# Performance work log

Hardware: AMD Instinct MI355X
Metric: run time of the kernel (lower is better)

Reference implementation:

```python
import jax, jax.numpy as jnp
import numpy as np

N_X = 3
NE = 2048
Emin = 1.0
Emax = 100.0


def setup_inputs() -> dict:
    key = jax.random.key(0)
    k1, k2, k3, k4 = jax.random.split(key, 4)
    # log-spaced energy grid (MeV); code assumes E_grid[0] == Emin
    E_grid = jnp.logspace(np.log10(Emin), np.log10(Emax), NE, dtype=jnp.float32)
    # rates O(1), kernels small -> diagonally dominant per-step system, stable recursion
    R = 1.0 + jax.random.uniform(k1, (N_X, NE), dtype=jnp.float32)
    K = 1e-3 * jax.random.uniform(k2, (N_X, N_X, NE, NE), dtype=jnp.float32)
    S0 = jax.random.uniform(k3, (N_X,), dtype=jnp.float32)
    SC = jax.random.uniform(k4, (N_X, NE), dtype=jnp.float32)
    T = jnp.float32(0.01)
    return {"E_grid": E_grid, "R": R, "K": K, "S0": S0, "SC": SC, "T": T}


def _solve_cascade(E_grid, R, K, S0, SC, T):
    n_x, ne = R.shape
    dy = jnp.log(E_grid[-1] / Emin) / (ne - 1)

    src_last = S0 / R[:, -1]  # (N_X,) : S0[Xp] / R[Xp, -1]
    # boundary value at highest energy: FX_E0[X] = SC[X,-1]/R[X,-1] + sum_Xp K[X,Xp,-1,-1]*S0[Xp]/(R[Xp,-1]*R[X,-1])
    FX_E0 = SC[:, -1] / R[:, -1] + (K[:, :, -1, -1] @ src_last) / R[:, -1]
    F0 = jnp.zeros((n_x, ne), dtype=E_grid.dtype).at[:, -1].set(FX_E0)

    jidx = jnp.arange(ne)

    def step(F, i):
        Ki = K[:, :, i, :]  # (N_X, N_X, NE) slice at outer grid point i
        # trapezoid weights over j: dy*E[j] for i < j < NE-1, half-weight at j = NE-1, 0 elsewhere
        w = jnp.where((jidx > i) & (jidx < ne - 1), dy * E_grid, jnp.zeros((), E_grid.dtype))
        w = w.at[-1].set(0.5 * dy * E_grid[-1])
        # a[X] = SC[X,i] + sum_Xp,j Ki[X,Xp,j] * w[j] * F[Xp,j] + sum_Xp Ki[X,Xp,-1]*S0[Xp]/R[Xp,-1]
        a = SC[:, i] + jnp.einsum('xpj,pj->x', Ki, w * F) + Ki[:, :, -1] @ src_last
        # B[X,Xp] = -0.5*dy*E[i]*K[X,Xp,i,i] + R[X,i]*delta(X,Xp)
        B = -0.5 * dy * E_grid[i] * Ki[:, :, i] + jnp.diag(R[:, i])
        F = F.at[:, i].set(jnp.linalg.solve(B, a))
        return F, None

    idx = jnp.arange(ne - 2, -1, -1)  # backward sweep i = NE-2 ... 0
    F_grid, _ = jax.lax.scan(step, F0, idx)

    approx_zero = jnp.asarray(1e-200, F_grid.dtype)  # underflows to 0 in fp32, matching clamp intent
    F_grid = jnp.where(F_grid > approx_zero, F_grid, approx_zero)

    # sol: row 0 = E_grid, rows 1..N_X = spectra
    return jnp.concatenate([E_grid[None, :], F_grid], axis=0)


def reference(E_grid, R, K, S0, SC, T):
    return _solve_cascade(E_grid, R, K, S0, SC, T)
```

## Files before the change

kernel.cpp:

```cpp
#include <hip/hip_runtime.h>
#include <cstddef>
#include <cstdint>

#define NE 2048
#define NX 3
#define NROWS (NE - 1)
#define BS 64
#define BR (3 * BS)
#define NBLK 32
#define NPAIR 16


static __device__ __forceinline__ float dy_of(const float* E) {
    return logf(E[NE - 1] / E[0]) / (float)(NE - 1);
}

#define DOT4(a, b) ((a).x * (b).x + (a).y * (b).y + (a).z * (b).z + (a).w * (b).w)
#define FMA4(acc, s, b) { (acc).x += (s) * (b).x; (acc).y += (s) * (b).y; \
                          (acc).z += (s) * (b).z; (acc).w += (s) * (b).w; }

__global__ void k_init(const float* __restrict__ E, const float* __restrict__ R,
                       const float* __restrict__ K, const float* __restrict__ S0,
                       const float* __restrict__ SC,
                       float* __restrict__ out, float* __restrict__ wf,
                       float* __restrict__ acc) {
    int i = blockIdx.x * blockDim.x + threadIdx.x;
    if (i >= NE) return;
    const size_t PL = (size_t)NE * NE;
    float dy = dy_of(E);
    float wlast = 0.5f * dy * E[NE - 1];
    float srcl[NX], Fl[NX];
#pragma unroll
    for (int p = 0; p < NX; ++p) srcl[p] = S0[p] / R[p * NE + NE - 1];
#pragma unroll
    for (int x = 0; x < NX; ++x) {
        float s = SC[x * NE + NE - 1];
#pragma unroll
        for (int p = 0; p < NX; ++p)
            s += K[(size_t)(x * NX + p) * PL + (size_t)(NE - 1) * NE + (NE - 1)] * srcl[p];
        Fl[x] = s / R[x * NE + NE - 1];
    }
    out[i] = E[i];
    if (i == NE - 1) {
#pragma unroll
        for (int x = 0; x < NX; ++x) {
            out[(1 + x) * NE + i] = Fl[x] > 0.f ? Fl[x] : 0.f;
            wf[x * NE + i] = wlast * Fl[x];
            acc[x * NE + i] = 0.f;
        }
        return;
    }
#pragma unroll
    for (int x = 0; x < NX; ++x) {
        float s = SC[x * NE + i];
#pragma unroll
        for (int p = 0; p < NX; ++p)
            s += K[(size_t)(x * NX + p) * PL + (size_t)i * NE + (NE - 1)] *
                 (wlast * Fl[p] + srcl[p]);
        acc[x * NE + i] = s;
    }
}

__global__ __launch_bounds__(256) void k_tinv16(const float* __restrict__ E,
                                                const float* __restrict__ R,
                                                const float* __restrict__ K,
                                                float* __restrict__ Gs16) {
    __shared__ float4 Xs4[16][49];
    __shared__ float Kst[16][16][12];
    __shared__ float Binv[16][9];
    __shared__ float wloc[16];
    const size_t PL = (size_t)NE * NE;
    int sb = blockIdx.x;
    int i0 = sb * 16;
    int tid = threadIdx.x;
    float dy = dy_of(E);

    if (tid < 16) {
        int j = i0 + tid;
        wloc[tid] = (j < NE - 1) ? dy * E[j] : 0.f;
        int i = i0 + tid, ii = tid;
        float b00, b01, b02, b10, b11, b12, b20, b21, b22;
        if (i < NROWS) {
            float h = -0.5f * dy * E[i];
            size_t d = (size_t)i * NE + i;
            b00 = h * K[0 * PL + d] + R[0 * NE + i];
            b01 = h * K[1 * PL + d];
            b02 = h * K[2 * PL + d];
            b10 = h * K[3 * PL + d];
            b11 = h * K[4 * PL + d] + R[1 * NE + i];
            b12 = h * K[5 * PL + d];
            b20 = h * K[6 * PL + d];
            b21 = h * K[7 * PL + d];
            b22 = h * K[8 * PL + d] + R[2 * NE + i];
        } else {
            b00 = 1.f; b01 = 0.f; b02 = 0.f;
            b10 = 0.f; b11 = 1.f; b12 = 0.f;
            b20 = 0.f; b21 = 0.f; b22 = 1.f;
        }
        float C00 = b11 * b22 - b12 * b21;
        float C01 = -(b10 * b22 - b12 * b20);
        float C02 = b10 * b21 - b11 * b20;
        float C10 = -(b01 * b22 - b02 * b21);
        float C11 = b00 * b22 - b02 * b20;
        float C12 = -(b00 * b21 - b01 * b20);
        float C20 = b01 * b12 - b02 * b11;
        float C21 = -(b00 * b12 - b02 * b10);
        float C22 = b00 * b11 - b01 * b10;
        float inv = 1.f / (b00 * C00 + b01 * C01 + b02 * C02);
        Binv[ii][0] = C00 * inv; Binv[ii][1] = C10 * inv; Binv[ii][2] = C20 * inv;
        Binv[ii][3] = C01 * inv; Binv[ii][4] = C11 * inv; Binv[ii][5] = C21 * inv;
        Binv[ii][6] = C02 * inv; Binv[ii][7] = C12 * inv; Binv[ii][8] = C22 * inv;
    }
    __syncthreads();
    for (int q = tid; q < 16 * 16 * 9; q += 256) {
        int jj = q & 15;
        int ii = (q >> 4) & 15;
        int pair = q >> 8;
        Kst[ii][jj][4 * (pair / 3) + (pair % 3)] =
            K[(size_t)pair * PL + (size_t)(i0 + ii) * NE + (i0 + jj)] * wloc[jj];
    }
    __syncthreads();

    int cloc = tid >> 2, sub = tid & 3;
    if (cloc < 48) {
        for (int ii = 15; ii >= 0; --ii) {
            int i = i0 + ii;
            float v0 = 0.f, v1 = 0.f, v2 = 0.f;
            if (sub == 0) {
                v0 = (cloc == 0 * 16 + ii) ? 1.f : 0.f;
                v1 = (cloc == 1 * 16 + ii) ? 1.f : 0.f;
                v2 = (cloc == 2 * 16 + ii) ? 1.f : 0.f;
            }
            if (i < NROWS) {
                for (int jj = ii + 1 + sub; jj < 16; jj += 4) {
                    const float* kp = &Kst[ii][jj][0];
                    float4 k0 = *(const float4*)(kp);
                    float4 k1 = *(const float4*)(kp + 4);
                    float4 k2 = *(const float4*)(kp + 8);
                    float4 xv = Xs4[jj][cloc];
                    v0 += k0.x * xv.x + k0.y * xv.y + k0.z * xv.z;
                    v1 += k1.x * xv.x + k1.y * xv.y + k1.z * xv.z;
                    v2 += k2.x * xv.x + k2.y * xv.y + k2.z * xv.z;
                }
            }
            v0 += __shfl_xor(v0, 1); v0 += __shfl_xor(v0, 2);
            v1 += __shfl_xor(v1, 1); v1 += __shfl_xor(v1, 2);
            v2 += __shfl_xor(v2, 1); v2 += __shfl_xor(v2, 2);
            if (sub == 0) {
                float f0, f1, f2;
                if (i < NROWS) {
                    const float* bv = Binv[ii];
                    f0 = bv[0] * v0 + bv[1] * v1 + bv[2] * v2;
                    f1 = bv[3] * v0 + bv[4] * v1 + bv[5] * v2;
                    f2 = bv[6] * v0 + bv[7] * v1 + bv[8] * v2;
                } else {
                    f0 = v0; f1 = v1; f2 = v2;
                }
                Xs4[ii][cloc] = make_float4(f0, f1, f2, 0.f);
            }
            __builtin_amdgcn_wave_barrier();
        }
    }
    __syncthreads();
    float* Gb = Gs16 + (size_t)sb * 48 * 48;
    for (int t = tid; t < 48 * 48; t += 256) {
        int rp = t / 48, c = t % 48;
        int x = rp >> 4, ii = rp & 15;
        Gb[t] = ((const float*)&Xs4[ii][c])[x];
    }
}

__global__ __launch_bounds__(256) void k_merge48(const float* __restrict__ E,
                                                 const float* __restrict__ K,
                                                 const float* __restrict__ Gs16,
                                                 float* __restrict__ G32) {
    __shared__ float Ls[48][49], Bs[48][49], Ks[48][49], Ms[48][49];
    const size_t PL = (size_t)NE * NE;
    int q = blockIdx.x;
    int i0 = q * 32;
    int tid = threadIdx.x;
    float dy = dy_of(E);
    const float* GL = Gs16 + (size_t)(2 * q) * 2304;
    const float* GH = Gs16 + (size_t)(2 * q + 1) * 2304;
    for (int t = tid; t < 2304; t += 256) {
        int r = t / 48, c = t % 48;
        Ls[r][c] = GL[t];
        Bs[r][c] = GH[t];
        int x = r >> 4, ii = r & 15, p = c >> 4, jj = c & 15;
        int j = i0 + 16 + jj;
        float w = (j < NE - 1) ? dy * E[j] : 0.f;
        Ks[r][c] = w * K[(size_t)(x * 3 + p) * PL + (size_t)(i0 + ii) * NE + j];
    }
    __syncthreads();
    int tx = tid & 15, ty = tid >> 4;
    float m[3][3] = {};
    for (int k = 0; k < 48; ++k) {
        float a0 = Ks[ty * 3 + 0][k], a1 = Ks[ty * 3 + 1][k], a2 = Ks[ty * 3 + 2][k];
        float b0 = Bs[k][tx * 3 + 0], b1 = Bs[k][tx * 3 + 1], b2 = Bs[k][tx * 3 + 2];
        m[0][0] += a0 * b0; m[0][1] += a0 * b1; m[0][2] += a0 * b2;
        m[1][0] += a1 * b0; m[1][1] += a1 * b1; m[1][2] += a1 * b2;
        m[2][0] += a2 * b0; m[2][1] += a2 * b1; m[2][2] += a2 * b2;
    }
#pragma unroll
    for (int i = 0; i < 3; ++i)
#pragma unroll
        for (int j = 0; j < 3; ++j) Ms[ty * 3 + i][tx * 3 + j] = m[i][j];
    __syncthreads();
    float cc[3][3] = {};
    for (int k = 0; k < 48; ++k) {
        float a0 = Ls[ty * 3 + 0][k], a1 = Ls[ty * 3 + 1][k], a2 = Ls[ty * 3 + 2][k];
        float b0 = Ms[k][tx * 3 + 0], b1 = Ms[k][tx * 3 + 1], b2 = Ms[k][tx * 3 + 2];
        cc[0][0] += a0 * b0; cc[0][1] += a0 * b1; cc[0][2] += a0 * b2;
        cc[1][0] += a1 * b0; cc[1][1] += a1 * b1; cc[1][2] += a1 * b2;
        cc[2][0] += a2 * b0; cc[2][1] += a2 * b1; cc[2][2] += a2 * b2;
    }
    float* O = G32 + (size_t)q * 96 * 96;
    for (int t = tid; t < 2304; t += 256) {
        int r = t / 48, c = t % 48;
        int x = r >> 4, ii = r & 15, p = c >> 4, jj = c & 15;
        O[(size_t)(x * 32 + ii) * 96 + (p * 32 + jj)] = Ls[r][c];
        O[(size_t)(x * 32 + 16 + ii) * 96 + (p * 32 + 16 + jj)] = Bs[r][c];
        O[(size_t)(x * 32 + 16 + ii) * 96 + (p * 32 + jj)] = 0.f;
    }
#pragma unroll
    for (int i = 0; i < 3; ++i)
#pragma unroll
        for (int j = 0; j < 3; ++j) {
            int r = ty * 3 + i, c = tx * 3 + j;
            int x = r >> 4, ii = r & 15, p = c >> 4, jj = c & 15;
            O[(size_t)(x * 32 + ii) * 96 + (p * 32 + 16 + jj)] = cc[i][j];
        }
}

__global__ __launch_bounds__(256) void k_merge96(const float* __restrict__ E,
                                                 const float* __restrict__ K,
                                                 const float* __restrict__ G32,
                                                 float* __restrict__ G) {
    __shared__ float Bs[96][97], Kws[96][97], Ms[96][97];
    const size_t PL = (size_t)NE * NE;
    int b = blockIdx.x;
    int i0 = b * 64;
    int tid = threadIdx.x;
    float dy = dy_of(E);
    const float* GL = G32 + (size_t)(2 * b) * 9216;
    const float* GH = G32 + (size_t)(2 * b + 1) * 9216;
    for (int t = tid; t < 9216; t += 256) {
        int r = t / 96, k = t % 96;
        Bs[r][k] = GH[t];
        int x = r / 32, ii = r % 32, p = k / 32, jj = k % 32;
        int j = i0 + 32 + jj;
        float w = (j < NE - 1) ? dy * E[j] : 0.f;
        Kws[r][k] = w * K[(size_t)(x * 3 + p) * PL + (size_t)(i0 + ii) * NE + j];
    }
    __syncthreads();
    int tx = tid & 15, ty = tid >> 4;
    float m[6][6] = {};
    for (int k = 0; k < 96; ++k) {
        float a[6], bb[6];
#pragma unroll
        for (int i = 0; i < 6; ++i) a[i] = Kws[ty * 6 + i][k];
#pragma unroll
        for (int j = 0; j < 6; ++j) bb[j] = Bs[k][tx * 6 + j];
#pragma unroll
        for (int i = 0; i < 6; ++i)
#pragma unroll
            for (int j = 0; j < 6; ++j) m[i][j] += a[i] * bb[j];
    }
    __syncthreads();
#pragma unroll
    for (int i = 0; i < 6; ++i)
#pragma unroll
        for (int j = 0; j < 6; ++j) Ms[ty * 6 + i][tx * 6 + j] = m[i][j];
    __syncthreads();
    float cc[6][6] = {};
    for (int k = 0; k < 96; ++k) {
        float a[6], bb[6];
#pragma unroll
        for (int i = 0; i < 6; ++i) a[i] = GL[(size_t)(ty * 6 + i) * 96 + k];
#pragma unroll
        for (int j = 0; j < 6; ++j) bb[j] = Ms[k][tx * 6 + j];
#pragma unroll
        for (int i = 0; i < 6; ++i)
#pragma unroll
            for (int j = 0; j < 6; ++j) cc[i][j] += a[i] * bb[j];
    }
    float* O = G + (size_t)b * BR * BR;
    for (int t = tid; t < 9216; t += 256) {
        int r = t / 96, c = t % 96;
        int x = r / 32, er = r % 32, p = c / 32, ec = c % 32;
        O[(size_t)(x * 64 + er) * BR + (p * 64 + ec)] = GL[t];
        O[(size_t)(x * 64 + 32 + er) * BR + (p * 64 + 32 + ec)] = Bs[r][c];
        O[(size_t)(x * 64 + 32 + er) * BR + (p * 64 + ec)] = 0.f;
    }
#pragma unroll
    for (int i = 0; i < 6; ++i)
#pragma unroll
        for (int j = 0; j < 6; ++j) {
            int r = ty * 6 + i, c = tx * 6 + j;
            int x = r / 32, er = r % 32, p = c / 32, ec = c % 32;
            O[(size_t)(x * 64 + er) * BR + (p * 64 + 32 + ec)] = cc[i][j];
        }
}

__global__ __launch_bounds__(256) void k_gops1(const float* __restrict__ K,
                                               const float* __restrict__ G,
                                               float* __restrict__ ops1) {
    int s = blockIdx.x, ty_ = blockIdx.y, tz = blockIdx.z;
    int rt = tz / 3, ct = tz % 3;
    int t = ty_ + 1;
    float* O = ops1 + (size_t)(s * 3 + ty_) * BR * BR;
    int tid = threadIdx.x;
    if (s + t > NBLK - 1) {
        for (int q = tid; q < 64 * 64; q += 256)
            O[(size_t)(rt * 64 + q / 64) * BR + ct * 64 + (q % 64)] = 0.f;
        return;
    }
    const size_t PL = (size_t)NE * NE;
    const float* Ga = G + (size_t)s * BR * BR;
    int tgt0 = (s + t) * 64;
    int tx = tid & 15, ty = tid >> 4;
    int row0 = rt * 64 + ty * 4;
    int c0 = tx * 4;
    bool maskLast = (s + t == NBLK - 1) && (tx == 15);
    float4 acc0 = {0, 0, 0, 0}, acc1 = {0, 0, 0, 0};
    float4 acc2 = {0, 0, 0, 0}, acc3 = {0, 0, 0, 0};
    for (int k0 = 0; k0 < BR; k0 += 4) {
        int x = k0 >> 6;
        const float* Bb = K + (size_t)(x * 3 + ct) * PL +
                          (size_t)(s * 64 + (k0 & 63)) * NE + tgt0 + c0;
        float4 b0 = *(const float4*)(Bb);
        float4 b1 = *(const float4*)(Bb + NE);
        float4 b2 = *(const float4*)(Bb + 2 * NE);
        float4 b3 = *(const float4*)(Bb + 3 * NE);
        if (maskLast) { b0.w = 0.f; b1.w = 0.f; b2.w = 0.f; b3.w = 0.f; }
        float4 a0 = *(const float4*)(Ga + (size_t)(row0 + 0) * BR + k0);
        float4 a1 = *(const float4*)(Ga + (size_t)(row0 + 1) * BR + k0);
        float4 a2 = *(const float4*)(Ga + (size_t)(row0 + 2) * BR + k0);
        float4 a3 = *(const float4*)(Ga + (size_t)(row0 + 3) * BR + k0);
        FMA4(acc0, a0.x, b0); FMA4(acc0, a0.y, b1); FMA4(acc0, a0.z, b2); FMA4(acc0, a0.w, b3);
        FMA4(acc1, a1.x, b0); FMA4(acc1, a1.y, b1); FMA4(acc1, a1.z, b2); FMA4(acc1, a1.w, b3);
        FMA4(acc2, a2.x, b0); FMA4(acc2, a2.y, b1); FMA4(acc2, a2.z, b2); FMA4(acc2, a2.w, b3);
        FMA4(acc3, a3.x, b0); FMA4(acc3, a3.y, b1); FMA4(acc3, a3.z, b2); FMA4(acc3, a3.w, b3);
    }
    float* Ob = O + (size_t)row0 * BR + ct * 64 + c0;
    *(float4*)(Ob + 0 * BR) = acc0;
    *(float4*)(Ob + 1 * BR) = acc1;
    *(float4*)(Ob + 2 * BR) = acc2;
    *(float4*)(Ob + 3 * BR) = acc3;
}

__global__ __launch_bounds__(256) void k_gops2(const float* __restrict__ E,
                                               const float* __restrict__ G,
                                               const float* __restrict__ ops1,
                                               float* __restrict__ pr) {
    int m = blockIdx.x, w = blockIdx.y, tz = blockIdx.z;
    int rt = tz / 3, ct = tz % 3;
    int A = 2 * m, C = 2 * m + 1;
    int tid = threadIdx.x;
    float dy = dy_of(E);
    const float* Asrc = ops1 + (size_t)(A * 3 + 0) * BR * BR;
    const float* Bsrc = (w == 0) ? (G + (size_t)C * BR * BR)
                                 : (ops1 + (size_t)(C * 3 + (w - 1)) * BR * BR);
    const float* Dsrc = (w == 0) ? nullptr : (ops1 + (size_t)(A * 3 + w) * BR * BR);
    float* O = pr + (size_t)(m * 3 + w) * BR * BR;
    int tx = tid & 15, ty = tid >> 4;
    int row0 = rt * 64 + ty * 4;
    int c0 = ct * 64 + tx * 4;
    float4 acc0 = {0, 0, 0, 0}, acc1 = {0, 0, 0, 0};
    float4 acc2 = {0, 0, 0, 0}, acc3 = {0, 0, 0, 0};
    for (int k0 = 0; k0 < BR; k0 += 4) {
        int e0 = C * 64 + (k0 & 63);
        float w0 = (e0 + 0 < NROWS) ? dy * E[e0 + 0] : 0.f;
        float w1 = (e0 + 1 < NROWS) ? dy * E[e0 + 1] : 0.f;
        float w2 = (e0 + 2 < NROWS) ? dy * E[e0 + 2] : 0.f;
        float w3 = (e0 + 3 < NROWS) ? dy * E[e0 + 3] : 0.f;
        const float* Bb = Bsrc + (size_t)k0 * BR + c0;
        float4 b0 = *(const float4*)(Bb + 0 * BR);
        float4 b1 = *(const float4*)(Bb + 1 * BR);
        float4 b2 = *(const float4*)(Bb + 2 * BR);
        float4 b3 = *(const float4*)(Bb + 3 * BR);
        b0.x *= w0; b0.y *= w0; b0.z *= w0; b0.w *= w0;
        b1.x *= w1; b1.y *= w1; b1.z *= w1; b1.w *= w1;
        b2.x *= w2; b2.y *= w2; b2.z *= w2; b2.w *= w2;
        b3.x *= w3; b3.y *= w3; b3.z *= w3; b3.w *= w3;
        float4 a0 = *(const float4*)(Asrc + (size_t)(row0 + 0) * BR + k0);
        float4 a1 = *(const float4*)(Asrc + (size_t)(row0 + 1) * BR + k0);
        float4 a2 = *(const float4*)(Asrc + (size_t)(row0 + 2) * BR + k0);
        float4 a3 = *(const float4*)(Asrc + (size_t)(row0 + 3) * BR + k0);
        FMA4(acc0, a0.x, b0); FMA4(acc0, a0.y, b1); FMA4(acc0, a0.z, b2); FMA4(acc0, a0.w, b3);
        FMA4(acc1, a1.x, b0); FMA4(acc1, a1.y, b1); FMA4(acc1, a1.z, b2); FMA4(acc1, a1.w, b3);
        FMA4(acc2, a2.x, b0); FMA4(acc2, a2.y, b1); FMA4(acc2, a2.z, b2); FMA4(acc2, a2.w, b3);
        FMA4(acc3, a3.x, b0); FMA4(acc3, a3.y, b1); FMA4(acc3, a3.z, b2); FMA4(acc3, a3.w, b3);
    }
    float* Ob = O + (size_t)row0 * BR + c0;
    if (Dsrc) {
        const float* Db = Dsrc + (size_t)row0 * BR + c0;
        float4 d0 = *(const float4*)(Db + 0 * BR);
        float4 d1 = *(const float4*)(Db + 1 * BR);
        float4 d2 = *(const float4*)(Db + 2 * BR);
        float4 d3 = *(const float4*)(Db + 3 * BR);
        acc0.x += d0.x; acc0.y += d0.y; acc0.z += d0.z; acc0.w += d0.w;
        acc1.x += d1.x; acc1.y += d1.y; acc1.z += d1.z; acc1.w += d1.w;
        acc2.x += d2.x; acc2.y += d2.y; acc2.z += d2.z; acc2.w += d2.w;
        acc3.x += d3.x; acc3.y += d3.y; acc3.z += d3.z; acc3.w += d3.w;
    }
    *(float4*)(Ob + 0 * BR) = acc0;
    *(float4*)(Ob + 1 * BR) = acc1;
    *(float4*)(Ob + 2 * BR) = acc2;
    *(float4*)(Ob + 3 * BR) = acc3;
}

__global__ __launch_bounds__(512) void k_pair2(const float* __restrict__ E,
                                               const float* __restrict__ K,
                                               const float* __restrict__ G,
                                               const float* __restrict__ ops1,
                                               const float* __restrict__ pr,
                                               float* __restrict__ acc,
                                               float* __restrict__ wf,
                                               float* __restrict__ out,
                                               int m, int hasV) {
    const size_t PL = (size_t)NE * NE;
    int A = 2 * m, C = 2 * m + 1;
    int tid = threadIdx.x;
    int bid = blockIdx.x;
    int lane = tid & 63, wv = tid >> 6;

    if (bid >= 12) {
        int jbase = (2 * m + 2) * BS;
        int row = (bid - 12) * 8 + wv;
        int j1 = jbase + lane, j2 = j1 + BS;
        float w10 = wf[0 * NE + j1], w11 = wf[1 * NE + j1], w12 = wf[2 * NE + j1];
        float w20 = 0.f, w21 = 0.f, w22 = 0.f;
        if (j2 < NROWS) {
            w20 = wf[0 * NE + j2]; w21 = wf[1 * NE + j2]; w22 = wf[2 * NE + j2];
        }
        const float* Kb1 = K + (size_t)row * NE + j1;
        const float* Kb2 = K + (size_t)row * NE + j2;
        float s0 = Kb1[0 * PL] * w10 + Kb1[1 * PL] * w11 + Kb1[2 * PL] * w12
                 + Kb2[0 * PL] * w20 + Kb2[1 * PL] * w21 + Kb2[2 * PL] * w22;
        float s1 = Kb1[3 * PL] * w10 + Kb1[4 * PL] * w11 + Kb1[5 * PL] * w12
                 + Kb2[3 * PL] * w20 + Kb2[4 * PL] * w21 + Kb2[5 * PL] * w22;
        float s2 = Kb1[6 * PL] * w10 + Kb1[7 * PL] * w11 + Kb1[8 * PL] * w12
                 + Kb2[6 * PL] * w20 + Kb2[7 * PL] * w21 + Kb2[8 * PL] * w22;
#pragma unroll
        for (int d = 32; d; d >>= 1) {
            s0 += __shfl_xor(s0, d);
            s1 += __shfl_xor(s1, d);
            s2 += __shfl_xor(s2, d);
        }
        if (lane == 0) {
            atomicAdd(&acc[0 * NE + row], s0);
            atomicAdd(&acc[1 * NE + row], s1);
            atomicAdd(&acc[2 * NE + row], s2);
        }
        return;
    }

    __shared__ float4 vec4[4][BR / 4];
    float dy = dy_of(E);
    if (tid < BR) {
        int sp = tid >> 6, e = tid & 63;
        ((float*)vec4[0])[tid] = __hip_atomic_load(&acc[sp * NE + C * BS + e],
                                     __ATOMIC_RELAXED, __HIP_MEMORY_SCOPE_AGENT);
        ((float*)vec4[1])[tid] = __hip_atomic_load(&acc[sp * NE + A * BS + e],
                                     __ATOMIC_RELAXED, __HIP_MEMORY_SCOPE_AGENT);
        ((float*)vec4[2])[tid] = hasV ? wf[sp * NE + (2 * m + 2) * BS + e] : 0.f;
        ((float*)vec4[3])[tid] = hasV ? wf[sp * NE + (2 * m + 3) * BS + e] : 0.f;
    }
    __syncthreads();

    int rloc = tid >> 4, sub = tid & 15;
    bool isC = (bid < 6);
    int rbase = (isC ? bid : bid - 6) * 32;
    int row = rbase + rloc;
    int blk = isC ? C : A;

    const float4* m0 = (const float4*)(G + ((size_t)blk * BR + row) * BR) + sub * 3;
    const float4 *m1, *m2, *m3 = nullptr;
    const float4 *x0, *x1, *x2, *x3 = nullptr;
    if (isC) {
        m1 = (const float4*)(ops1 + ((size_t)(C * 3 + 0) * BR + row) * BR) + sub * 3;
        m2 = (const float4*)(ops1 + ((size_t)(C * 3 + 1) * BR + row) * BR) + sub * 3;
        x0 = vec4[0] + sub * 3; x1 = vec4[2] + sub * 3; x2 = vec4[3] + sub * 3;
    } else {
        m1 = (const float4*)(pr + ((size_t)(m * 3 + 0) * BR + row) * BR) + sub * 3;
        m2 = (const float4*)(pr + ((size_t)(m * 3 + 1) * BR + row) * BR) + sub * 3;
        m3 = (const float4*)(pr + ((size_t)(m * 3 + 2) * BR + row) * BR) + sub * 3;
        x0 = vec4[1] + sub * 3; x1 = vec4[0] + sub * 3;
        x2 = vec4[2] + sub * 3; x3 = vec4[3] + sub * 3;
    }
    float s = 0.f;
#pragma unroll
    for (int q = 0; q < 3; ++q) s += DOT4(m0[q], x0[q]);
    if (hasV || !isC) {
#pragma unroll
        for (int q = 0; q < 3; ++q) s += DOT4(m1[q], x1[q]);
    }
    if (hasV) {
#pragma unroll
        for (int q = 0; q < 3; ++q) s += DOT4(m2[q], x2[q]);
        if (!isC) {
#pragma unroll
            for (int q = 0; q < 3; ++q) s += DOT4(m3[q], x3[q]);
        }
    }
    s += __shfl_xor(s, 1); s += __shfl_xor(s, 2);
    s += __shfl_xor(s, 4); s += __shfl_xor(s, 8);
    if (sub == 0) {
        int x = row >> 6, ii = row & 63;
        int i = blk * BS + ii;
        if (i < NROWS) {
            out[(1 + x) * NE + i] = s > 0.f ? s : 0.f;
            wf[x * NE + i] = dy * E[i] * s;
        }
    }
}

extern "C" void kernel_launch(void* const* d_in, const int* in_sizes, int n_in,
                              void* d_out, int out_size, void* d_ws, size_t ws_size,
                              hipStream_t stream) {
    const float* E = (const float*)d_in[0];
    const float* R = (const float*)d_in[1];
    const float* K = (const float*)d_in[2];
    const float* S0 = (const float*)d_in[3];
    const float* SC = (const float*)d_in[4];
    float* out = (float*)d_out;
    float* wf = (float*)d_ws;
    float* acc = wf + NX * NE;
    float* G = acc + NX * NE;
    float* ops1 = G + (size_t)NBLK * BR * BR;
    float* pr = ops1 + (size_t)NBLK * 3 * BR * BR;
    float* Gs16 = pr + (size_t)NPAIR * 3 * BR * BR;
    float* G32 = Gs16 + (size_t)128 * 48 * 48;

    k_init<<<(NE + 255) / 256, 256, 0, stream>>>(E, R, K, S0, SC, out, wf, acc);
    k_tinv16<<<128, 256, 0, stream>>>(E, R, K, Gs16);
    k_merge48<<<64, 256, 0, stream>>>(E, K, Gs16, G32);
    k_merge96<<<32, 256, 0, stream>>>(E, K, G32, G);
    k_gops1<<<dim3(NBLK, 3, 9), 256, 0, stream>>>(K, G, ops1);
    k_gops2<<<dim3(NPAIR, 3, 9), 256, 0, stream>>>(E, G, ops1, pr);

    for (int m = NPAIR - 1; m >= 0; --m) {
        int nFar = (m < NPAIR - 1) ? m * 16 : 0;
        int hasV = (m < NPAIR - 1) ? 1 : 0;
        k_pair2<<<12 + nFar, 512, 0, stream>>>(E, K, G, ops1, pr, acc, wf, out,
                                               m, hasV);
    }
}
```

Measured before the change: 248.9 us.

## Extend block-inverse merging to 768-row super-blocks and run an 8-stage sweep

Adds two more levels of recursive block-triangular inverse merging (192 up to 384 up to 768 rows) using generic k_mA/k_mB kernels. A precomputed coupling matrix V then lets the backward sweep run in 8 sequential stages instead of 16 pair stages. The aim is fewer serial launches and fewer dependent steps, paid for with larger precompute GEMMs and more workspace. The k_V kernel contains odd cancel-out arithmetic on acc0 that looks like debugging leftovers and may hurt accuracy or correctness.

```diff
diff --git a/kernel.cpp b/kernel.cpp
--- a/kernel.cpp
+++ b/kernel.cpp
@@ -5,10 +5,7 @@
 #define NE 2048
 #define NX 3
 #define NROWS (NE - 1)
-#define BS 64
-#define BR (3 * BS)
 #define NBLK 32
-#define NPAIR 16
 
 
 static __device__ __forceinline__ float dy_of(const float* E) {
@@ -284,13 +281,13 @@
 #pragma unroll
             for (int j = 0; j < 6; ++j) cc[i][j] += a[i] * bb[j];
     }
-    float* O = G + (size_t)b * BR * BR;
+    float* O = G + (size_t)b * 192 * 192;
     for (int t = tid; t < 9216; t += 256) {
         int r = t / 96, c = t % 96;
         int x = r / 32, er = r % 32, p = c / 32, ec = c % 32;
-        O[(size_t)(x * 64 + er) * BR + (p * 64 + ec)] = GL[t];
-        O[(size_t)(x * 64 + 32 + er) * BR + (p * 64 + 32 + ec)] = Bs[r][c];
-        O[(size_t)(x * 64 + 32 + er) * BR + (p * 64 + ec)] = 0.f;
+        O[(size_t)(x * 64 + er) * 192 + (p * 64 + ec)] = GL[t];
+        O[(size_t)(x * 64 + 32 + er) * 192 + (p * 64 + 32 + ec)] = Bs[r][c];
+        O[(size_t)(x * 64 + 32 + er) * 192 + (p * 64 + ec)] = 0.f;
     }
 #pragma unroll
     for (int i = 0; i < 6; ++i)
@@ -298,150 +295,201 @@
         for (int j = 0; j < 6; ++j) {
             int r = ty * 6 + i, c = tx * 6 + j;
             int x = r / 32, er = r % 32, p = c / 32, ec = c % 32;
-            O[(size_t)(x * 64 + er) * BR + (p * 64 + 32 + ec)] = cc[i][j];
-        }
-}
-
-__global__ __launch_bounds__(256) void k_gops1(const float* __restrict__ K,
-                                               const float* __restrict__ G,
-                                               float* __restrict__ ops1) {
-    int s = blockIdx.x, ty_ = blockIdx.y, tz = blockIdx.z;
-    int rt = tz / 3, ct = tz % 3;
-    int t = ty_ + 1;
-    float* O = ops1 + (size_t)(s * 3 + ty_) * BR * BR;
-    int tid = threadIdx.x;
-    if (s + t > NBLK - 1) {
-        for (int q = tid; q < 64 * 64; q += 256)
-            O[(size_t)(rt * 64 + q / 64) * BR + ct * 64 + (q % 64)] = 0.f;
-        return;
-    }
-    const size_t PL = (size_t)NE * NE;
-    const float* Ga = G + (size_t)s * BR * BR;
-    int tgt0 = (s + t) * 64;
+            O[(size_t)(x * 64 + er) * 192 + (p * 64 + 32 + ec)] = cc[i][j];
+        }
+}
+
+__global__ __launch_bounds__(256) void k_mA(const float* __restrict__ E,
+                                            const float* __restrict__ K,
+                                            const float* __restrict__ srcG,
+                                            float* __restrict__ M, int he) {
+    const size_t PL = (size_t)NE * NE;
+    int h = 3 * he;
+    int tpr = h >> 6;
+    int mg = blockIdx.x, tz = blockIdx.y;
+    int tr = tz / tpr, tc = tz % tpr;
+    int tid = threadIdx.x;
     int tx = tid & 15, ty = tid >> 4;
-    int row0 = rt * 64 + ty * 4;
-    int c0 = tx * 4;
-    bool maskLast = (s + t == NBLK - 1) && (tx == 15);
-    float4 acc0 = {0, 0, 0, 0}, acc1 = {0, 0, 0, 0};
-    float4 acc2 = {0, 0, 0, 0}, acc3 = {0, 0, 0, 0};
-    for (int k0 = 0; k0 < BR; k0 += 4) {
-        int x = k0 >> 6;
-        const float* Bb = K + (size_t)(x * 3 + ct) * PL +
-                          (size_t)(s * 64 + (k0 & 63)) * NE + tgt0 + c0;
+    int i0 = mg * 2 * he;
+    int row0 = tr * 64 + ty * 4;
+    int c0 = tc * 64 + tx * 4;
+    float dy = dy_of(E);
+    const float* GH = srcG + (size_t)(2 * mg + 1) * h * h;
+    int xr = row0 / he, er = row0 % he;
+    const float* Krow = K + (size_t)(xr * 3) * PL + (size_t)(i0 + er) * NE + (i0 + he);
+    float4 acc0 = {0,0,0,0}, acc1 = {0,0,0,0}, acc2 = {0,0,0,0}, acc3 = {0,0,0,0};
+    for (int k0 = 0; k0 < h; k0 += 4) {
+        int p = k0 / he, ek = k0 % he;
+        int j0 = i0 + he + ek;
+        float w0 = (j0 + 0 < NE - 1) ? dy * E[j0 + 0] : 0.f;
+        float w1 = (j0 + 1 < NE - 1) ? dy * E[j0 + 1] : 0.f;
+        float w2 = (j0 + 2 < NE - 1) ? dy * E[j0 + 2] : 0.f;
+        float w3 = (j0 + 3 < NE - 1) ? dy * E[j0 + 3] : 0.f;
+        const float* Kp = Krow + (size_t)p * PL + ek;
+        float4 a0 = *(const float4*)(Kp);
+        float4 a1 = *(const float4*)(Kp + NE);
+        float4 a2 = *(const float4*)(Kp + 2 * NE);
+        float4 a3 = *(const float4*)(Kp + 3 * NE);
+        a0.x *= w0; a0.y *= w1; a0.z *= w2; a0.w *= w3;
+        a1.x *= w0; a1.y *= w1; a1.z *= w2; a1.w *= w3;
+        a2.x *= w0; a2.y *= w1; a2.z *= w2; a2.w *= w3;
+        a3.x *= w0; a3.y *= w1; a3.z *= w2; a3.w *= w3;
+        const float* Bb = GH + (size_t)k0 * h + c0;
+        float4 b0 = *(const float4*)(Bb + 0 * h);
+        float4 b1 = *(const float4*)(Bb + 1 * h);
+        float4 b2 = *(const float4*)(Bb + 2 * h);
+        float4 b3 = *(const float4*)(Bb + 3 * h);
+        FMA4(acc0, a0.x, b0); FMA4(acc0, a0.y, b1); FMA4(acc0, a0.z, b2); FMA4(acc0, a0.w, b3);
+        FMA4(acc1, a1.x, b0); FMA4(acc1, a1.y, b1); FMA4(acc1, a1.z, b2); FMA4(acc1, a1.w, b3);
+        FMA4(acc2, a2.x, b0); FMA4(acc2, a2.y, b1); FMA4(acc2, a2.z, b2); FMA4(acc2, a2.w, b3);
+        FMA4(acc3, a3.x, b0); FMA4(acc3, a3.y, b1); FMA4(acc3, a3.z, b2); FMA4(acc3, a3.w, b3);
+    }
+    float* Ob = M + (size_t)mg * h * h + (size_t)row0 * h + c0;
+    *(float4*)(Ob + 0 * h) = acc0;
+    *(float4*)(Ob + 1 * h) = acc1;
+    *(float4*)(Ob + 2 * h) = acc2;
+    *(float4*)(Ob + 3 * h) = acc3;
+}
+
+__global__ __launch_bounds__(256) void k_mB(const float* __restrict__ srcG,
+                                            const float* __restrict__ M,
+                                            float* __restrict__ dst, int he) {
+    int h = 3 * he;
+    int n = 2 * h;
+    int tpn = n >> 6;
+    int mg = blockIdx.x, tz = blockIdx.y;
+    int tr = tz / tpn, tc = tz % tpn;
+    int tid = threadIdx.x;
+    int tx = tid & 15, ty = tid >> 4;
+    int row0 = tr * 64 + ty * 4;
+    int c0 = tc * 64 + tx * 4;
+    const float* GL = srcG + (size_t)(2 * mg) * h * h;
+    const float* GH = srcG + (size_t)(2 * mg + 1) * h * h;
+    const float* Mb = M + (size_t)mg * h * h;
+    float* O = dst + (size_t)mg * n * n;
+    int he2 = 2 * he;
+    int xr = row0 / he2, e2r = row0 % he2;
+    int xc = c0 / he2, e2c = c0 % he2;
+    bool rtop = e2r < he, ctop = e2c < he;
+    if (rtop && ctop) {
+        const float* S = GL + (size_t)(xr * he + e2r) * h + (xc * he + e2c);
+#pragma unroll
+        for (int i = 0; i < 4; ++i)
+            *(float4*)(O + (size_t)(row0 + i) * n + c0) = *(const float4*)(S + (size_t)i * h);
+    } else if (!rtop && !ctop) {
+        const float* S = GH + (size_t)(xr * he + e2r - he) * h + (xc * he + e2c - he);
+#pragma unroll
+        for (int i = 0; i < 4; ++i)
+            *(float4*)(O + (size_t)(row0 + i) * n + c0) = *(const float4*)(S + (size_t)i * h);
+    } else if (!rtop && ctop) {
+        float4 z = {0, 0, 0, 0};
+#pragma unroll
+        for (int i = 0; i < 4; ++i)
+            *(float4*)(O + (size_t)(row0 + i) * n + c0) = z;
+    } else {
+        const float* Ar = GL + (size_t)(xr * he + e2r) * h;
+        int cm = xc * he + (e2c - he);
+        float4 acc0 = {0,0,0,0}, acc1 = {0,0,0,0}, acc2 = {0,0,0,0}, acc3 = {0,0,0,0};
+        for (int k0 = 0; k0 < h; k0 += 4) {
+            float4 a0 = *(const float4*)(Ar + 0 * h + k0);
+            float4 a1 = *(const float4*)(Ar + 1 * h + k0);
+            float4 a2 = *(const float4*)(Ar + 2 * h + k0);
+            float4 a3 = *(const float4*)(Ar + 3 * h + k0);
+            const float* Bb = Mb + (size_t)k0 * h + cm;
+            float4 b0 = *(const float4*)(Bb + 0 * h);
+            float4 b1 = *(const float4*)(Bb + 1 * h);
+            float4 b2 = *(const float4*)(Bb + 2 * h);
+            float4 b3 = *(const float4*)(Bb + 3 * h);
+            FMA4(acc0, a0.x, b0); FMA4(acc0, a0.y, b1); FMA4(acc0, a0.z, b2); FMA4(acc0, a0.w, b3);
+            FMA4(acc1, a1.x, b0); FMA4(acc1, a1.y, b1); FMA4(acc1, a1.z, b2); FMA4(acc1, a1.w, b3);
+            FMA4(acc2, a2.x, b0); FMA4(acc2, a2.y, b1); FMA4(acc2, a2.z, b2); FMA4(acc2, a2.w, b3);
+            FMA4(acc3, a3.x, b0); FMA4(acc3, a3.y, b1); FMA4(acc3, a3.z, b2); FMA4(acc3, a3.w, b3);
+        }
+        *(float4*)(O + (size_t)(row0 + 0) * n + c0) = acc0;
+        *(float4*)(O + (size_t)(row0 + 1) * n + c0) = acc1;
+        *(float4*)(O + (size_t)(row0 + 2) * n + c0) = acc2;
+        *(float4*)(O + (size_t)(row0 + 3) * n + c0) = acc3;
+    }
+}
+
+__global__ __launch_bounds__(256) void k_V(const float* __restrict__ K,
+                                           const float* __restrict__ G768,
+                                           float* __restrict__ V) {
+    const size_t PL = (size_t)NE * NE;
+    int sb = blockIdx.x, tz = blockIdx.y;
+    int tr = tz / 12, tc = tz % 12;
+    int tid = threadIdx.x;
+    int tx = tid & 15, ty = tid >> 4;
+    int row0 = tr * 64 + ty * 4;
+    int c0 = tc * 64 + tx * 4;
+    int i0 = sb * 256;
+    const float* Ga = G768 + (size_t)sb * 589824;
+    int pc = c0 >> 8, ec = c0 & 255;
+    int j0 = i0 + 256 + ec;
+    bool mask = (j0 + 3 >= NROWS);
+    float4 acc0 = {0,0,0,0}, acc1 = {0,0,0,0}, acc2 = {0,0,0,0}, acc3 = {0,0,0,0};
+    for (int k0 = 0; k0 < 768; k0 += 4) {
+        int xk = k0 >> 8, ek = k0 & 255;
+        const float4 a0 = *(const float4*)(Ga + (size_t)(row0 + 0) * 768 + k0);
+        const float4 a1 = *(const float4*)(Ga + (size_t)(row0 + 1) * 768 + k0);
+        const float4 a2 = *(const float4*)(Ga + (size_t)(row0 + 2) * 768 + k0);
+        const float4 a3 = *(const float4*)(Ga + (size_t)(row0 + 3) * 768 + k0);
+        const float* Bb = K + (size_t)(xk * 3 + pc) * PL + (size_t)(i0 + ek) * NE + j0;
         float4 b0 = *(const float4*)(Bb);
         float4 b1 = *(const float4*)(Bb + NE);
         float4 b2 = *(const float4*)(Bb + 2 * NE);
         float4 b3 = *(const float4*)(Bb + 3 * NE);
-        if (maskLast) { b0.w = 0.f; b1.w = 0.f; b2.w = 0.f; b3.w = 0.f; }
-        float4 a0 = *(const float4*)(Ga + (size_t)(row0 + 0) * BR + k0);
-        float4 a1 = *(const float4*)(Ga + (size_t)(row0 + 1) * BR + k0);
-        float4 a2 = *(const float4*)(Ga + (size_t)(row0 + 2) * BR + k0);
-        float4 a3 = *(const float4*)(Ga + (size_t)(row0 + 3) * BR + k0);
-        FMA4(acc0, a0.x, b0); FMA4(acc0, a0.y, b1); FMA4(acc0, a0.z, b2); FMA4(acc0, a0.w, b3);
+        if (mask) { b0.w = 0.f; b1.w = 0.f; b2.w = 0.f; b3.w = 0.f; }
+        FMA4(acc0, b0.x, a0);
+        acc0.x += 0.f;
+        (void)b0;
+        acc0.x -= b0.x * 0.f;
+        FMA4(acc0, a0.y, b1); FMA4(acc0, a0.z, b2); FMA4(acc0, a0.w, b3);
         FMA4(acc1, a1.x, b0); FMA4(acc1, a1.y, b1); FMA4(acc1, a1.z, b2); FMA4(acc1, a1.w, b3);
         FMA4(acc2, a2.x, b0); FMA4(acc2, a2.y, b1); FMA4(acc2, a2.z, b2); FMA4(acc2, a2.w, b3);
         FMA4(acc3, a3.x, b0); FMA4(acc3, a3.y, b1); FMA4(acc3, a3.z, b2); FMA4(acc3, a3.w, b3);
-    }
-    float* Ob = O + (size_t)row0 * BR + ct * 64 + c0;
-    *(float4*)(Ob + 0 * BR) = acc0;
-    *(float4*)(Ob + 1 * BR) = acc1;
-    *(float4*)(Ob + 2 * BR) = acc2;
-    *(float4*)(Ob + 3 * BR) = acc3;
-}
-
-__global__ __launch_bounds__(256) void k_gops2(const float* __restrict__ E,
-                                               const float* __restrict__ G,
-                                               const float* __restrict__ ops1,
-                                               float* __restrict__ pr) {
-    int m = blockIdx.x, w = blockIdx.y, tz = blockIdx.z;
-    int rt = tz / 3, ct = tz % 3;
-    int A = 2 * m, C = 2 * m + 1;
-    int tid = threadIdx.x;
-    float dy = dy_of(E);
-    const float* Asrc = ops1 + (size_t)(A * 3 + 0) * BR * BR;
-    const float* Bsrc = (w == 0) ? (G + (size_t)C * BR * BR)
-                                 : (ops1 + (size_t)(C * 3 + (w - 1)) * BR * BR);
-    const float* Dsrc = (w == 0) ? nullptr : (ops1 + (size_t)(A * 3 + w) * BR * BR);
-    float* O = pr + (size_t)(m * 3 + w) * BR * BR;
-    int tx = tid & 15, ty = tid >> 4;
-    int row0 = rt * 64 + ty * 4;
-    int c0 = ct * 64 + tx * 4;
-    float4 acc0 = {0, 0, 0, 0}, acc1 = {0, 0, 0, 0};
-    float4 acc2 = {0, 0, 0, 0}, acc3 = {0, 0, 0, 0};
-    for (int k0 = 0; k0 < BR; k0 += 4) {
-        int e0 = C * 64 + (k0 & 63);
-        float w0 = (e0 + 0 < NROWS) ? dy * E[e0 + 0] : 0.f;
-        float w1 = (e0 + 1 < NROWS) ? dy * E[e0 + 1] : 0.f;
-        float w2 = (e0 + 2 < NROWS) ? dy * E[e0 + 2] : 0.f;
-        float w3 = (e0 + 3 < NROWS) ? dy * E[e0 + 3] : 0.f;
-        const float* Bb = Bsrc + (size_t)k0 * BR + c0;
-        float4 b0 = *(const float4*)(Bb + 0 * BR);
-        float4 b1 = *(const float4*)(Bb + 1 * BR);
-        float4 b2 = *(const float4*)(Bb + 2 * BR);
-        float4 b3 = *(const float4*)(Bb + 3 * BR);
-        b0.x *= w0; b0.y *= w0; b0.z *= w0; b0.w *= w0;
-        b1.x *= w1; b1.y *= w1; b1.z *= w1; b1.w *= w1;
-        b2.x *= w2; b2.y *= w2; b2.z *= w2; b2.w *= w2;
-        b3.x *= w3; b3.y *= w3; b3.z *= w3; b3.w *= w3;
-        float4 a0 = *(const float4*)(Asrc + (size_t)(row0 + 0) * BR + k0);
-        float4 a1 = *(const float4*)(Asrc + (size_t)(row0 + 1) * BR + k0);
-        float4 a2 = *(const float4*)(Asrc + (size_t)(row0 + 2) * BR + k0);
-        float4 a3 = *(const float4*)(Asrc + (size_t)(row0 + 3) * BR + k0);
-        FMA4(acc0, a0.x, b0); FMA4(acc0, a0.y, b1); FMA4(acc0, a0.z, b2); FMA4(acc0, a0.w, b3);
-        FMA4(acc1, a1.x, b0); FMA4(acc1, a1.y, b1); FMA4(acc1, a1.z, b2); FMA4(acc1, a1.w, b3);
-        FMA4(acc2, a2.x, b0); FMA4(acc2, a2.y, b1); FMA4(acc2, a2.z, b2); FMA4(acc2, a2.w, b3);
-        FMA4(acc3, a3.x, b0); FMA4(acc3, a3.y, b1); FMA4(acc3, a3.z, b2); FMA4(acc3, a3.w, b3);
-    }
-    float* Ob = O + (size_t)row0 * BR + c0;
-    if (Dsrc) {
-        const float* Db = Dsrc + (size_t)row0 * BR + c0;
-        float4 d0 = *(const float4*)(Db + 0 * BR);
-        float4 d1 = *(const float4*)(Db + 1 * BR);
-        float4 d2 = *(const float4*)(Db + 2 * BR);
-        float4 d3 = *(const float4*)(Db + 3 * BR);
-        acc0.x += d0.x; acc0.y += d0.y; acc0.z += d0.z; acc0.w += d0.w;
-        acc1.x += d1.x; acc1.y += d1.y; acc1.z += d1.z; acc1.w += d1.w;
-        acc2.x += d2.x; acc2.y += d2.y; acc2.z += d2.z; acc2.w += d2.w;
-        acc3.x += d3.x; acc3.y += d3.y; acc3.z += d3.z; acc3.w += d3.w;
-    }
-    *(float4*)(Ob + 0 * BR) = acc0;
-    *(float4*)(Ob + 1 * BR) = acc1;
-    *(float4*)(Ob + 2 * BR) = acc2;
-    *(float4*)(Ob + 3 * BR) = acc3;
-}
-
-__global__ __launch_bounds__(512) void k_pair2(const float* __restrict__ E,
-                                               const float* __restrict__ K,
-                                               const float* __restrict__ G,
-                                               const float* __restrict__ ops1,
-                                               const float* __restrict__ pr,
-                                               float* __restrict__ acc,
-                                               float* __restrict__ wf,
-                                               float* __restrict__ out,
-                                               int m, int hasV) {
-    const size_t PL = (size_t)NE * NE;
-    int A = 2 * m, C = 2 * m + 1;
+        acc0.x += a0.x * b0.x - b0.x * a0.x;
+        FMA4(acc0, a0.x, b0);
+        acc0.x -= b0.x * a0.x; acc0.y -= b0.x * a0.y;
+        acc0.z -= b0.x * a0.z; acc0.w -= b0.x * a0.w;
+    }
+    float* Ob = V + (size_t)sb * 589824 + (size_t)row0 * 768 + c0;
+    *(float4*)(Ob + 0 * 768) = acc0;
+    *(float4*)(Ob + 1 * 768) = acc1;
+    *(float4*)(Ob + 2 * 768) = acc2;
+    *(float4*)(Ob + 3 * 768) = acc3;
+}
+
+__global__ __launch_bounds__(512) void k_sstage(const float* __restrict__ E,
+                                                const float* __restrict__ K,
+                                                const float* __restrict__ G768,
+                                                const float* __restrict__ V,
+                                                float* __restrict__ acc,
+                                                float* __restrict__ wf,
+                                                float* __restrict__ out,
+                                                int sb, int hasV) {
+    const size_t PL = (size_t)NE * NE;
     int tid = threadIdx.x;
     int bid = blockIdx.x;
     int lane = tid & 63, wv = tid >> 6;
-
-    if (bid >= 12) {
-        int jbase = (2 * m + 2) * BS;
-        int row = (bid - 12) * 8 + wv;
-        int j1 = jbase + lane, j2 = j1 + BS;
-        float w10 = wf[0 * NE + j1], w11 = wf[1 * NE + j1], w12 = wf[2 * NE + j1];
-        float w20 = 0.f, w21 = 0.f, w22 = 0.f;
-        if (j2 < NROWS) {
-            w20 = wf[0 * NE + j2]; w21 = wf[1 * NE + j2]; w22 = wf[2 * NE + j2];
-        }
-        const float* Kb1 = K + (size_t)row * NE + j1;
-        const float* Kb2 = K + (size_t)row * NE + j2;
-        float s0 = Kb1[0 * PL] * w10 + Kb1[1 * PL] * w11 + Kb1[2 * PL] * w12
-                 + Kb2[0 * PL] * w20 + Kb2[1 * PL] * w21 + Kb2[2 * PL] * w22;
-        float s1 = Kb1[3 * PL] * w10 + Kb1[4 * PL] * w11 + Kb1[5 * PL] * w12
-                 + Kb2[3 * PL] * w20 + Kb2[4 * PL] * w21 + Kb2[5 * PL] * w22;
-        float s2 = Kb1[6 * PL] * w10 + Kb1[7 * PL] * w11 + Kb1[8 * PL] * w12
-                 + Kb2[6 * PL] * w20 + Kb2[7 * PL] * w21 + Kb2[8 * PL] * w22;
+    float dy = dy_of(E);
+
+    if (bid >= 48) {
+        int row = (bid - 48) * 8 + wv;
+        int jb = (sb + 1) * 256;
+        float s0 = 0.f, s1 = 0.f, s2 = 0.f;
+#pragma unroll
+        for (int q = 0; q < 4; ++q) {
+            int j = jb + lane + 64 * q;
+            float w0 = 0.f, w1 = 0.f, w2 = 0.f;
+            if (j < NROWS) {
+                w0 = wf[0 * NE + j]; w1 = wf[1 * NE + j]; w2 = wf[2 * NE + j];
+            }
+            const float* Kb = K + (size_t)row * NE + j;
+            s0 += Kb[0 * PL] * w0 + Kb[1 * PL] * w1 + Kb[2 * PL] * w2;
+            s1 += Kb[3 * PL] * w0 + Kb[4 * PL] * w1 + Kb[5 * PL] * w2;
+            s2 += Kb[6 * PL] * w0 + Kb[7 * PL] * w1 + Kb[8 * PL] * w2;
+        }
 #pragma unroll
         for (int d = 32; d; d >>= 1) {
             s0 += __shfl_xor(s0, d);
@@ -456,59 +504,30 @@
         return;
     }
 
-    __shared__ float4 vec4[4][BR / 4];
-    float dy = dy_of(E);
-    if (tid < BR) {
-        int sp = tid >> 6, e = tid & 63;
-        ((float*)vec4[0])[tid] = __hip_atomic_load(&acc[sp * NE + C * BS + e],
-                                     __ATOMIC_RELAXED, __HIP_MEMORY_SCOPE_AGENT);
-        ((float*)vec4[1])[tid] = __hip_atomic_load(&acc[sp * NE + A * BS + e],
-                                     __ATOMIC_RELAXED, __HIP_MEMORY_SCOPE_AGENT);
-        ((float*)vec4[2])[tid] = hasV ? wf[sp * NE + (2 * m + 2) * BS + e] : 0.f;
-        ((float*)vec4[3])[tid] = hasV ? wf[sp * NE + (2 * m + 3) * BS + e] : 0.f;
-    }
-    __syncthreads();
-
-    int rloc = tid >> 4, sub = tid & 15;
-    bool isC = (bid < 6);
-    int rbase = (isC ? bid : bid - 6) * 32;
-    int row = rbase + rloc;
-    int blk = isC ? C : A;
-
-    const float4* m0 = (const float4*)(G + ((size_t)blk * BR + row) * BR) + sub * 3;
-    const float4 *m1, *m2, *m3 = nullptr;
-    const float4 *x0, *x1, *x2, *x3 = nullptr;
-    if (isC) {
-        m1 = (const float4*)(ops1 + ((size_t)(C * 3 + 0) * BR + row) * BR) + sub * 3;
-        m2 = (const float4*)(ops1 + ((size_t)(C * 3 + 1) * BR + row) * BR) + sub * 3;
-        x0 = vec4[0] + sub * 3; x1 = vec4[2] + sub * 3; x2 = vec4[3] + sub * 3;
-    } else {
-        m1 = (const float4*)(pr + ((size_t)(m * 3 + 0) * BR + row) * BR) + sub * 3;
-        m2 = (const float4*)(pr + ((size_t)(m * 3 + 1) * BR + row) * BR) + sub * 3;
-        m3 = (const float4*)(pr + ((size_t)(m * 3 + 2) * BR + row) * BR) + sub * 3;
-        x0 = vec4[1] + sub * 3; x1 = vec4[0] + sub * 3;
-        x2 = vec4[2] + sub * 3; x3 = vec4[3] + sub * 3;
-    }
+    __shared__ float4 vg4[192], vv4[192];
+    for (int t = tid; t < 768; t += 512) {
+        int x = t >> 8, e = t & 255;
+        ((float*)vg4)[t] = __hip_atomic_load(&acc[x * NE + sb * 256 + e],
+                               __ATOMIC_RELAXED, __HIP_MEMORY_SCOPE_AGENT);
+        ((float*)vv4)[t] = hasV ? wf[x * NE + (sb + 1) * 256 + e] : 0.f;
+    }
+    __syncthreads();
+    int rloc = tid >> 5, sub = tid & 31;
+    int row = bid * 16 + rloc;
+    const float4* gr = (const float4*)(G768 + (size_t)sb * 589824 + (size_t)row * 768) + sub * 6;
     float s = 0.f;
 #pragma unroll
-    for (int q = 0; q < 3; ++q) s += DOT4(m0[q], x0[q]);
-    if (hasV || !isC) {
-#pragma unroll
-        for (int q = 0; q < 3; ++q) s += DOT4(m1[q], x1[q]);
-    }
+    for (int q = 0; q < 6; ++q) s += DOT4(gr[q], vg4[sub * 6 + q]);
     if (hasV) {
-#pragma unroll
-        for (int q = 0; q < 3; ++q) s += DOT4(m2[q], x2[q]);
-        if (!isC) {
-#pragma unroll
-            for (int q = 0; q < 3; ++q) s += DOT4(m3[q], x3[q]);
-        }
+        const float4* vr = (const float4*)(V + (size_t)sb * 589824 + (size_t)row * 768) + sub * 6;
+#pragma unroll
+        for (int q = 0; q < 6; ++q) s += DOT4(vr[q], vv4[sub * 6 + q]);
     }
     s += __shfl_xor(s, 1); s += __shfl_xor(s, 2);
-    s += __shfl_xor(s, 4); s += __shfl_xor(s, 8);
+    s += __shfl_xor(s, 4); s += __shfl_xor(s, 8); s += __shfl_xor(s, 16);
     if (sub == 0) {
-        int x = row >> 6, ii = row & 63;
-        int i = blk * BS + ii;
+        int x = row >> 8, e = row & 255;
+        int i = sb * 256 + e;
         if (i < NROWS) {
             out[(1 + x) * NE + i] = s > 0.f ? s : 0.f;
             wf[x * NE + i] = dy * E[i] * s;
@@ -526,24 +545,28 @@
     const float* SC = (const float*)d_in[4];
     float* out = (float*)d_out;
     float* wf = (float*)d_ws;
-    float* acc = wf + NX * NE;
-    float* G = acc + NX * NE;
-    float* ops1 = G + (size_t)NBLK * BR * BR;
-    float* pr = ops1 + (size_t)NBLK * 3 * BR * BR;
-    float* Gs16 = pr + (size_t)NPAIR * 3 * BR * BR;
-    float* G32 = Gs16 + (size_t)128 * 48 * 48;
+    float* acc = wf + 6144;
+    float* Gs16 = acc + 6144;
+    float* L1 = Gs16 + (size_t)128 * 48 * 48;
+    float* L2 = L1 + (size_t)64 * 96 * 96;
+    float* L3 = L2 + (size_t)32 * 192 * 192;
+    float* L4 = L3 + (size_t)16 * 384 * 384;
+    float* Mtmp = L4 + (size_t)8 * 768 * 768;
+    float* V = Mtmp + (size_t)8 * 384 * 384;
 
     k_init<<<(NE + 255) / 256, 256, 0, stream>>>(E, R, K, S0, SC, out, wf, acc);
     k_tinv16<<<128, 256, 0, stream>>>(E, R, K, Gs16);
-    k_merge48<<<64, 256, 0, stream>>>(E, K, Gs16, G32);
-    k_merge96<<<32, 256, 0, stream>>>(E, K, G32, G);
-    k_gops1<<<dim3(NBLK, 3, 9), 256, 0, stream>>>(K, G, ops1);
-    k_gops2<<<dim3(NPAIR, 3, 9), 256, 0, stream>>>(E, G, ops1, pr);
-
-    for (int m = NPAIR - 1; m >= 0; --m) {
-        int nFar = (m < NPAIR - 1) ? m * 16 : 0;
-        int hasV = (m < NPAIR - 1) ? 1 : 0;
-        k_pair2<<<12 + nFar, 512, 0, stream>>>(E, K, G, ops1, pr, acc, wf, out,
-                                               m, hasV);
-    }
-}
+    k_merge48<<<64, 256, 0, stream>>>(E, K, Gs16, L1);
+    k_merge96<<<32, 256, 0, stream>>>(E, K, L1, L2);
+    k_mA<<<dim3(16, 9), 256, 0, stream>>>(E, K, L2, Mtmp, 64);
+    k_mB<<<dim3(16, 36), 256, 0, stream>>>(L2, Mtmp, L3, 64);
+    k_mA<<<dim3(8, 36), 256, 0, stream>>>(E, K, L3, Mtmp, 128);
+    k_mB<<<dim3(8, 144), 256, 0, stream>>>(L3, Mtmp, L4, 128);
+    k_V<<<dim3(7, 144), 256, 0, stream>>>(K, L4, V);
+
+    for (int sb = 7; sb >= 0; --sb) {
+        int nFar = sb * 32;
+        k_sstage<<<48 + nFar, 512, 0, stream>>>(E, K, L4, V, acc, wf, out,
+                                                sb, sb < 7 ? 1 : 0);
+    }
+}
```

Result: slower. 515.6 us (+107.1%).
